# Optimization experiments

Hardware: AMD Instinct MI355X
Metric: run time of the kernel (lower is better)

Reference implementation:

```python
import jax, jax.numpy as jnp
import numpy as np

N = 50000          # nodes
E = 1_600_000      # edges
IN = 256           # in_channels
C = 32             # hidden_channels (per-head width)
HEADS = 4
BN_EPS = 1e-5


def setup_inputs() -> dict:
    key = jax.random.key(0)
    ks = jax.random.split(key, 32)
    g = lambda k, shp, s=0.1: (jax.random.normal(k, shp, jnp.float32) * s)
    inp = {
        "x": jax.random.normal(ks[0], (N, IN), jnp.float32),
        "edge_index": jax.random.randint(ks[1], (2, E), 0, N, jnp.int64),
        "edge_attr": jax.random.uniform(ks[2], (E, 1), jnp.float32),
        # conv1 (GATConv in=IN, out=C, heads=HEADS, edge_dim=1)
        "W1": g(ks[3], (IN, HEADS * C)),
        "as1": g(ks[4], (HEADS, C)),
        "ad1": g(ks[5], (HEADS, C)),
        "We1": g(ks[6], (1, HEADS * C)),
        "ae1": g(ks[7], (HEADS, C)),
        "b1": jnp.zeros((HEADS * C,), jnp.float32),
        # bn1 (eval mode, running_mean=0, running_var=1)
        "g1": jnp.ones((HEADS * C,), jnp.float32),
        "be1": jnp.zeros((HEADS * C,), jnp.float32),
        # conv2 (GATConv in=HEADS*C, out=C, heads=1, concat=False, edge_dim=1)
        "W2": g(ks[8], (HEADS * C, C)),
        "as2": g(ks[9], (1, C)),
        "ad2": g(ks[10], (1, C)),
        "We2": g(ks[11], (1, C)),
        "ae2": g(ks[12], (1, C)),
        "b2": jnp.zeros((C,), jnp.float32),
        # bn2
        "g2": jnp.ones((C,), jnp.float32),
        "be2": jnp.zeros((C,), jnp.float32),
        # classifier: Linear(C,16) -> ReLU -> Linear(16,2)
        "Wc1": g(ks[13], (C, 16)),
        "bc1": jnp.zeros((16,), jnp.float32),
        "Wc2": g(ks[14], (16, 2)),
        "bc2": jnp.zeros((2,), jnp.float32),
        "Wr1": g(ks[15], (C, 16)),
        "br1": jnp.zeros((16,), jnp.float32),
        "Wr2": g(ks[16], (16, 1)),
        "br2": jnp.zeros((1,), jnp.float32),
    }
    return inp


def _gat_conv(x, src, dst, eattr, W, a_src, a_dst, We, a_e, bias, heads, c, concat):
    n = x.shape[0]
    xs = (x @ W).reshape(n, heads, c)                       # [N,H,C]
    al_s = (xs * a_src).sum(-1)                              # [N,H]
    al_d = (xs * a_dst).sum(-1)                              # [N,H]
    ee = (eattr @ We).reshape(-1, heads, c)                  # [E,H,C]
    al_e = (ee * a_e).sum(-1)                                # [E,H]
    alpha = al_s[src] + al_d[dst] + al_e                     # [E,H]
    alpha = jax.nn.leaky_relu(alpha, 0.2)
    # segment softmax over destination node
    mx = jax.ops.segment_max(alpha, dst, num_segments=n)
    ex = jnp.exp(alpha - mx[dst])
    den = jax.ops.segment_sum(ex, dst, num_segments=n)
    a = ex / (den[dst] + 1e-16)                              # [E,H]
    out = jax.ops.segment_sum(xs[src] * a[..., None], dst, num_segments=n)  # [N,H,C]
    out = out.reshape(n, heads * c) if concat else out.mean(axis=1)
    return out + bias


def _add_self_loops(src, dst, eattr, n):
    loop = jnp.arange(n, dtype=src.dtype)
    fill = jnp.broadcast_to(eattr.mean(axis=0, keepdims=True), (n, eattr.shape[1]))
    return (jnp.concatenate([src, loop]), jnp.concatenate([dst, loop]),
            jnp.concatenate([eattr, fill], axis=0))


def _bn_eval(x, gamma, beta):
    # running_mean=0, running_var=1 (fresh BatchNorm1d, eval mode)
    return x * (gamma / jnp.sqrt(1.0 + BN_EPS)) + beta


def reference(x, edge_index, edge_attr, W1, as1, ad1, We1, ae1, b1, g1, be1,
              W2, as2, ad2, We2, ae2, b2, g2, be2,
              Wc1, bc1, Wc2, bc2, Wr1, br1, Wr2, br2):
    n = x.shape[0]
    src, dst, ea = _add_self_loops(edge_index[0], edge_index[1], edge_attr, n)
    h = _gat_conv(x, src, dst, ea, W1, as1, ad1, We1, ae1, b1, HEADS, C, True)
    h = jax.nn.elu(_bn_eval(h, g1, be1))
    h = _gat_conv(h, src, dst, ea, W2, as2, ad2, We2, ae2, b2, 1, C, False)
    h = jax.nn.elu(_bn_eval(h, g2, be2))
    cls = jax.nn.relu(h @ Wc1 + bc1) @ Wc2 + bc2             # [N,2]
    reg = (jax.nn.relu(h @ Wr1 + br1) @ Wr2 + br2)[:, 0]     # [N]
    return cls, reg, h
```

## Files before the change

### kernel.cpp

```cpp
#include <hip/hip_runtime.h>
#include <cstdint>
#include <cstddef>

#define NN 50000
#define EE 1600000
#define IN_DIM 256
#define HC 128
#define CD 32
#define BN_RS 0.9999950000374997f

#define CAP1 128
#define CAP2 128
#define NBKT 196
#define S1_B 782
#define HIST_B 320
#define G1_B 782

typedef __attribute__((ext_vector_type(8))) short short8;
typedef __attribute__((ext_vector_type(4))) float f32x4;

__device__ __forceinline__ float lrelu(float a) { return a > 0.f ? a : 0.2f * a; }
__device__ __forceinline__ float elu(float a) { return a > 0.f ? a : (__expf(a) - 1.f); }

__device__ __forceinline__ unsigned short f2bf(float f) {
    unsigned int u = __float_as_uint(f);
    unsigned int r = (u + 0x7FFFu + ((u >> 16) & 1u)) >> 16;
    return (unsigned short)r;
}
__device__ __forceinline__ float bf2f(unsigned short b) {
    return __uint_as_float(((unsigned int)b) << 16);
}
__device__ __forceinline__ float2 bf2f2(unsigned int p) {
    float2 r;
    r.x = __uint_as_float(p << 16);
    r.y = __uint_as_float(p & 0xFFFF0000u);
    return r;
}
__device__ __forceinline__ void unpack_edge(unsigned long long p, int& s, float& eav) {
    s = (int)(unsigned int)(p & 0xFFFFFFFFull);
    eav = __uint_as_float((unsigned int)(p >> 32));
}

__device__ __forceinline__ int block_excl_scan_256(int v, int tid, int* wsum) {
    int lane = tid & 63, wv = tid >> 6;
    int x = v;
    #pragma unroll
    for (int off = 1; off < 64; off <<= 1) {
        int y = __shfl_up(x, off);
        if (lane >= off) x += y;
    }
    if (lane == 63) wsum[wv] = x;
    __syncthreads();
    int wpre = 0;
    #pragma unroll
    for (int w = 0; w < 4; w++)
        if (w < wv) wpre += wsum[w];
    return wpre + x - v;
}

__global__ __launch_bounds__(256) void k0_prep(const float* __restrict__ W1,
                                               const float* __restrict__ W2,
                                               const float* __restrict__ We1,
                                               const float* __restrict__ ae1,
                                               const float* __restrict__ We2,
                                               const float* __restrict__ ae2,
                                               unsigned short* __restrict__ W1hi,
                                               unsigned short* __restrict__ W1lo,
                                               unsigned short* __restrict__ W2hi,
                                               unsigned short* __restrict__ W2lo,
                                               float* __restrict__ consts,
                                               int* __restrict__ bucketHist) {
    int blk = blockIdx.x;
    int tid = threadIdx.x;
    if (blk < 16) {
        int t = blk * 256 + tid;
        int lane = t & 63;
        int kt = (t >> 6) & 7;
        int nt = t >> 9;
        int kbase = kt * 32 + (lane >> 4) * 8;
        int col = nt * 16 + (lane & 15);
        size_t obase = (size_t)t * 8;
        #pragma unroll
        for (int j = 0; j < 8; j++) {
            float w = W1[(size_t)(kbase + j) * HC + col];
            unsigned short h = f2bf(w);
            W1hi[obase + j] = h;
            W1lo[obase + j] = f2bf(w - bf2f(h));
        }
    } else if (blk < 18) {
        int t = (blk - 16) * 256 + tid;
        int lane = t & 63;
        int kt = (t >> 6) & 3;
        int nt = t >> 8;
        int kbase = kt * 32 + (lane >> 4) * 8;
        int col = nt * 16 + (lane & 15);
        size_t obase = (size_t)t * 8;
        #pragma unroll
        for (int j = 0; j < 8; j++) {
            float w = W2[(size_t)(kbase + j) * CD + col];
            unsigned short h = f2bf(w);
            W2hi[obase + j] = h;
            W2lo[obase + j] = f2bf(w - bf2f(h));
        }
    } else {
        if (tid < NBKT) bucketHist[tid] = 0;
        if (tid == 200) consts[0] = 0.f;
        if (tid < 4) {
            float s = 0.f;
            for (int c = 0; c < 32; c++) s += We1[tid * 32 + c] * ae1[tid * 32 + c];
            consts[2 + tid] = s;
        } else if (tid == 4) {
            float s = 0.f;
            for (int c = 0; c < 32; c++) s += We2[c] * ae2[c];
            consts[6] = s;
        }
    }
}

__global__ __launch_bounds__(256) void kA_hist_gemm1(const int* __restrict__ ei,
                                                     const float* __restrict__ ea,
                                                     const float* __restrict__ x,
                                                     const unsigned short* __restrict__ Whi,
                                                     const unsigned short* __restrict__ Wlo,
                                                     int* __restrict__ bucketHist,
                                                     float* __restrict__ easum,
                                                     unsigned short* __restrict__ xs1b) {
    __shared__ int h[256];
    int tid = threadIdx.x;
    if (blockIdx.x < HIST_B) {
        h[tid] = 0;
        __syncthreads();
        float s = 0.f;
        for (int i = blockIdx.x * 256 + tid; i < EE; i += HIST_B * 256) {
            atomicAdd(&h[ei[EE + i] >> 8], 1);
            s += ea[i];
        }
        __syncthreads();
        if (tid < NBKT && h[tid] > 0) atomicAdd(&bucketHist[tid], h[tid]);
        #pragma unroll
        for (int off = 32; off > 0; off >>= 1) s += __shfl_xor(s, off);
        if ((tid & 63) == 0) atomicAdd(easum, s);
    } else {
        int lane = tid & 63, wv = tid >> 6;
        int row0 = (blockIdx.x - HIST_B) * 64 + wv * 16;
        if (row0 >= NN) return;
        int m = lane & 15;
        int q = lane >> 4;
        f32x4 acc[8];
        #pragma unroll
        for (int nt = 0; nt < 8; nt++) acc[nt] = {0.f, 0.f, 0.f, 0.f};
        const float* xrow = x + (size_t)(row0 + m) * IN_DIM + q * 8;
        #pragma unroll
        for (int kt = 0; kt < 8; kt++) {
            float4 v0 = *(const float4*)(xrow + kt * 32);
            float4 v1 = *(const float4*)(xrow + kt * 32 + 4);
            float vv[8] = {v0.x, v0.y, v0.z, v0.w, v1.x, v1.y, v1.z, v1.w};
            short8 ahi, alo;
            #pragma unroll
            for (int j = 0; j < 8; j++) {
                unsigned short hh = f2bf(vv[j]);
                ahi[j] = (short)hh;
                alo[j] = (short)f2bf(vv[j] - bf2f(hh));
            }
            #pragma unroll
            for (int nt = 0; nt < 8; nt++) {
                size_t fb = ((size_t)(nt * 8 + kt) * 64 + lane) * 8;
                short8 bhi = *(const short8*)(Whi + fb);
                short8 blo = *(const short8*)(Wlo + fb);
                acc[nt] = __builtin_amdgcn_mfma_f32_16x16x32_bf16(ahi, bhi, acc[nt], 0, 0, 0);
                acc[nt] = __builtin_amdgcn_mfma_f32_16x16x32_bf16(ahi, blo, acc[nt], 0, 0, 0);
                acc[nt] = __builtin_amdgcn_mfma_f32_16x16x32_bf16(alo, bhi, acc[nt], 0, 0, 0);
            }
        }
        #pragma unroll
        for (int nt = 0; nt < 8; nt++) {
            #pragma unroll
            for (int reg = 0; reg < 4; reg++) {
                int row = row0 + q * 4 + reg;
                xs1b[(size_t)row * HC + nt * 16 + m] = f2bf(acc[nt][reg]);
            }
        }
    }
}

__global__ void bucket_scan(const int* __restrict__ bucketHist,
                            int* __restrict__ bucketBase,
                            int* __restrict__ bucketCursor,
                            int* __restrict__ indptr,
                            float* __restrict__ consts) {
    __shared__ int wsum[4];
    int tid = threadIdx.x;
    int v = (tid < NBKT) ? bucketHist[tid] : 0;
    int excl = block_excl_scan_256(v, tid, wsum);
    if (tid <= NBKT) bucketBase[tid] = (tid == NBKT) ? EE : excl;
    if (tid < NBKT) bucketCursor[tid] = excl;
    if (tid == 0) { indptr[NN] = EE; consts[1] = consts[0] / (float)EE; }
}

__global__ __launch_bounds__(256) void kB_stage1_al1(const int* __restrict__ ei,
                                                     const float* __restrict__ ea,
                                                     int* __restrict__ bucketCursor,
                                                     int* __restrict__ Adst,
                                                     int* __restrict__ Asrc,
                                                     float* __restrict__ Aea,
                                                     const unsigned short* __restrict__ xs1b,
                                                     const float* __restrict__ as1,
                                                     const float* __restrict__ ad1,
                                                     float* __restrict__ als,
                                                     float* __restrict__ ald) {
    __shared__ int cnt[256];
    __shared__ int basel[256];
    __shared__ int gbase[256];
    __shared__ int wsum[4];
    __shared__ int sdst[2048];
    __shared__ int ssrc[2048];
    __shared__ float sea[2048];
    int tid = threadIdx.x;
    if (blockIdx.x < S1_B) {
        int base = blockIdx.x * 2048;
        cnt[tid] = 0;
        __syncthreads();
        int d[8], s[8], r[8], bk[8];
        float e[8];
        #pragma unroll
        for (int k = 0; k < 8; k++) {
            int i = base + k * 256 + tid;
            if (i < EE) {
                d[k] = ei[EE + i];
                s[k] = ei[i];
                e[k] = ea[i];
                bk[k] = d[k] >> 8;
                r[k] = atomicAdd(&cnt[bk[k]], 1);
            } else d[k] = -1;
        }
        __syncthreads();
        int v = cnt[tid];
        int excl = block_excl_scan_256(v, tid, wsum);
        basel[tid] = excl;
        if (tid < NBKT) gbase[tid] = atomicAdd(&bucketCursor[tid], v);
        __syncthreads();
        #pragma unroll
        for (int k = 0; k < 8; k++) {
            if (d[k] >= 0) {
                int slot = basel[bk[k]] + r[k];
                sdst[slot] = d[k];
                ssrc[slot] = s[k];
                sea[slot] = e[k];
            }
        }
        __syncthreads();
        int total = basel[255] + cnt[255];
        for (int slot = tid; slot < total; slot += 256) {
            int dd = sdst[slot];
            int b = dd >> 8;
            int pos = gbase[b] + (slot - basel[b]);
            Adst[pos] = dd;
            Asrc[pos] = ssrc[slot];
            Aea[pos] = sea[slot];
        }
    } else {
        int t = (blockIdx.x - S1_B) * 256 + tid;
        if (t < NN * 4) {
            int hh = t & 3;
            const unsigned int* xp = (const unsigned int*)(xs1b + (size_t)t * 32);
            const float* ap = as1 + hh * 32;
            const float* dp = ad1 + hh * 32;
            float s = 0.f, d = 0.f;
            #pragma unroll
            for (int q = 0; q < 16; q++) {
                float2 v = bf2f2(xp[q]);
                s += v.x * ap[q * 2] + v.y * ap[q * 2 + 1];
                d += v.x * dp[q * 2] + v.y * dp[q * 2 + 1];
            }
            als[t] = s;
            ald[t] = d;
        }
    }
}

__global__ __launch_bounds__(1024) void stage2_kernel(const int* __restrict__ bucketBase,
                                                      const int* __restrict__ Adst,
                                                      const int* __restrict__ Asrc,
                                                      const float* __restrict__ Aea,
                                                      int* __restrict__ indptr,
                                                      unsigned long long* __restrict__ edgedat) {
    __shared__ int cnt[256];
    __shared__ int dbase[256];
    int tid = threadIdx.x;
    int b = blockIdx.x;
    int start = bucketBase[b], end = bucketBase[b + 1];
    if (tid < 256) cnt[tid] = 0;
    __syncthreads();
    for (int i = start + tid; i < end; i += 1024) atomicAdd(&cnt[Adst[i] & 255], 1);
    __syncthreads();
    if (tid < 64) {
        int b4 = tid * 4;
        int c0 = cnt[b4], c1 = cnt[b4 + 1], c2 = cnt[b4 + 2], c3 = cnt[b4 + 3];
        int t = c0 + c1 + c2 + c3;
        int x = t;
        #pragma unroll
        for (int off = 1; off < 64; off <<= 1) {
            int y = __shfl_up(x, off);
            if (tid >= off) x += y;
        }
        int e0 = x - t;
        dbase[b4] = e0;
        dbase[b4 + 1] = e0 + c0;
        dbase[b4 + 2] = e0 + c0 + c1;
        dbase[b4 + 3] = e0 + c0 + c1 + c2;
    }
    __syncthreads();
    if (tid < 256) {
        int n = b * 256 + tid;
        if (n < NN) indptr[n] = start + dbase[tid];
        cnt[tid] = 0;
    }
    __syncthreads();
    for (int i = start + tid; i < end; i += 1024) {
        int dl = Adst[i] & 255;
        int r = atomicAdd(&cnt[dl], 1);
        int pos = start + dbase[dl] + r;
        edgedat[pos] = (unsigned long long)(unsigned int)Asrc[i] |
                       ((unsigned long long)__float_as_uint(Aea[i]) << 32);
    }
}

__global__ __launch_bounds__(256) void gat1_agg(
    const unsigned short* __restrict__ xs1b, const float* __restrict__ als,
    const float* __restrict__ ald, const unsigned long long* __restrict__ edgedat,
    const int* __restrict__ indptr, const float* __restrict__ consts,
    const float* __restrict__ b1, const float* __restrict__ g1,
    const float* __restrict__ be1,
    unsigned short* __restrict__ h1hi, unsigned short* __restrict__ h1lo) {
    __shared__ float exbuf[4][CAP1 * 4];
    __shared__ int srcbuf[4][CAP1];
    int wv = threadIdx.x >> 6;
    int lane = threadIdx.x & 63;
    int n = blockIdx.x * 4 + wv;
    int start = indptr[n];
    int deg = indptr[n + 1] - start;
    float ea_mean = consts[1];
    float ce[4] = {consts[2], consts[3], consts[4], consts[5]};
    float4 a4d = *(const float4*)(ald + (size_t)n * 4);
    float aldh[4] = {a4d.x, a4d.y, a4d.z, a4d.w};
    float4 a4s = *(const float4*)(als + (size_t)n * 4);
    float alsn[4] = {a4s.x, a4s.y, a4s.z, a4s.w};
    float ex0[4], sm[4];
    #pragma unroll
    for (int h = 0; h < 4; h++) {
        ex0[h] = __expf(lrelu(alsn[h] + aldh[h] + ea_mean * ce[h]));
        sm[h] = 0.f;
    }
    const unsigned long long* edp = edgedat + start;
    for (int i = lane; i < deg; i += 64) {
        int s; float eav;
        unpack_edge(edp[i], s, eav);
        float4 v4 = *(const float4*)(als + (size_t)s * 4);
        float alv[4] = {v4.x, v4.y, v4.z, v4.w};
        bool st = (i < CAP1);
        if (st) srcbuf[wv][i] = s * HC;
        #pragma unroll
        for (int h = 0; h < 4; h++) {
            float exv = __expf(lrelu(alv[h] + aldh[h] + eav * ce[h]));
            if (st) exbuf[wv][i * 4 + h] = exv;
            sm[h] += exv;
        }
    }
    #pragma unroll
    for (int h = 0; h < 4; h++)
        for (int off = 32; off > 0; off >>= 1) sm[h] += __shfl_xor(sm[h], off);
    float inv[4];
    #pragma unroll
    for (int h = 0; h < 4; h++) inv[h] = 1.0f / (sm[h] + ex0[h] + 1e-16f);
    int mcap = deg < CAP1 ? deg : CAP1;
    for (int i = lane; i < mcap; i += 64) {
        #pragma unroll
        for (int h = 0; h < 4; h++) exbuf[wv][i * 4 + h] *= inv[h];
    }
    int c = lane * 2;
    int h = lane >> 4;
    float wsl = ex0[h] * inv[h];
    float2 vself = bf2f2(*(const unsigned int*)(xs1b + (size_t)n * HC + c));
    float accx = vself.x * wsl, accy = vself.y * wsl;
    int i = 0;
    for (; i + 4 <= mcap; i += 4) {
        float w0 = exbuf[wv][(i + 0) * 4 + h];
        float w1 = exbuf[wv][(i + 1) * 4 + h];
        float w2 = exbuf[wv][(i + 2) * 4 + h];
        float w3 = exbuf[wv][(i + 3) * 4 + h];
        int o0 = srcbuf[wv][i + 0], o1 = srcbuf[wv][i + 1];
        int o2 = srcbuf[wv][i + 2], o3 = srcbuf[wv][i + 3];
        float2 v0 = bf2f2(*(const unsigned int*)(xs1b + o0 + c));
        float2 v1 = bf2f2(*(const unsigned int*)(xs1b + o1 + c));
        float2 v2 = bf2f2(*(const unsigned int*)(xs1b + o2 + c));
        float2 v3 = bf2f2(*(const unsigned int*)(xs1b + o3 + c));
        accx += v0.x * w0; accy += v0.y * w0;
        accx += v1.x * w1; accy += v1.y * w1;
        accx += v2.x * w2; accy += v2.y * w2;
        accx += v3.x * w3; accy += v3.y * w3;
    }
    for (; i < mcap; i++) {
        float w0 = exbuf[wv][i * 4 + h];
        int o0 = srcbuf[wv][i];
        float2 v0 = bf2f2(*(const unsigned int*)(xs1b + o0 + c));
        accx += v0.x * w0; accy += v0.y * w0;
    }
    for (; i < deg; i++) {
        int s; float eav;
        unpack_edge(edp[i], s, eav);
        float a = lrelu(als[(size_t)s * 4 + h] + aldh[h] + eav * ce[h]);
        float w0 = __expf(a) * inv[h];
        float2 v0 = bf2f2(*(const unsigned int*)(xs1b + (size_t)s * HC + c));
        accx += v0.x * w0; accy += v0.y * w0;
    }
    float o0 = accx + b1[c];
    float o1 = accy + b1[c + 1];
    o0 = o0 * (g1[c] * BN_RS) + be1[c];
    o1 = o1 * (g1[c + 1] * BN_RS) + be1[c + 1];
    o0 = elu(o0);
    o1 = elu(o1);
    unsigned short h0 = f2bf(o0), h1v = f2bf(o1);
    unsigned short l0 = f2bf(o0 - bf2f(h0)), l1 = f2bf(o1 - bf2f(h1v));
    *(unsigned int*)(h1hi + (size_t)n * HC + c) = (unsigned int)h0 | ((unsigned int)h1v << 16);
    *(unsigned int*)(h1lo + (size_t)n * HC + c) = (unsigned int)l0 | ((unsigned int)l1 << 16);
}

__global__ __launch_bounds__(256) void gemm2_mfma(const unsigned short* __restrict__ h1hi,
                                                  const unsigned short* __restrict__ h1lo,
                                                  const unsigned short* __restrict__ W2hi,
                                                  const unsigned short* __restrict__ W2lo,
                                                  const float* __restrict__ as2,
                                                  const float* __restrict__ ad2,
                                                  unsigned short* __restrict__ xs2b,
                                                  float* __restrict__ als2,
                                                  float* __restrict__ ald2) {
    int tid = threadIdx.x;
    int lane = tid & 63, wv = tid >> 6;
    int row0 = blockIdx.x * 64 + wv * 16;
    if (row0 >= NN) return;
    int m = lane & 15, q = lane >> 4;
    f32x4 acc[2];
    acc[0] = {0.f, 0.f, 0.f, 0.f};
    acc[1] = {0.f, 0.f, 0.f, 0.f};
    const unsigned short* rhi = h1hi + (size_t)(row0 + m) * HC + q * 8;
    const unsigned short* rlo = h1lo + (size_t)(row0 + m) * HC + q * 8;
    #pragma unroll
    for (int kt = 0; kt < 4; kt++) {
        short8 ahi = *(const short8*)(rhi + kt * 32);
        short8 alo = *(const short8*)(rlo + kt * 32);
        #pragma unroll
        for (int nt = 0; nt < 2; nt++) {
            size_t fb = ((size_t)(nt * 4 + kt) * 64 + lane) * 8;
            short8 bhi = *(const short8*)(W2hi + fb);
            short8 blo = *(const short8*)(W2lo + fb);
            acc[nt] = __builtin_amdgcn_mfma_f32_16x16x32_bf16(ahi, bhi, acc[nt], 0, 0, 0);
            acc[nt] = __builtin_amdgcn_mfma_f32_16x16x32_bf16(ahi, blo, acc[nt], 0, 0, 0);
            acc[nt] = __builtin_amdgcn_mfma_f32_16x16x32_bf16(alo, bhi, acc[nt], 0, 0, 0);
        }
    }
    float a0 = as2[m], a1 = as2[m + 16];
    float d0 = ad2[m], d1 = ad2[m + 16];
    #pragma unroll
    for (int reg = 0; reg < 4; reg++) {
        int row = row0 + q * 4 + reg;
        xs2b[(size_t)row * CD + m]      = f2bf(acc[0][reg]);
        xs2b[(size_t)row * CD + 16 + m] = f2bf(acc[1][reg]);
        float s = acc[0][reg] * a0 + acc[1][reg] * a1;
        float d = acc[0][reg] * d0 + acc[1][reg] * d1;
        #pragma unroll
        for (int off = 1; off < 16; off <<= 1) {
            s += __shfl_xor(s, off);
            d += __shfl_xor(d, off);
        }
        if (m == 0) { als2[row] = s; ald2[row] = d; }
    }
}

__global__ __launch_bounds__(256) void gat2_agg(
    const unsigned short* __restrict__ xs2b, const float* __restrict__ als,
    const float* __restrict__ ald, const unsigned long long* __restrict__ edgedat,
    const int* __restrict__ indptr, const float* __restrict__ consts,
    const float* __restrict__ b2, const float* __restrict__ g2, const float* __restrict__ be2,
    const float* __restrict__ Wc1, const float* __restrict__ bc1,
    const float* __restrict__ Wc2, const float* __restrict__ bc2,
    const float* __restrict__ Wr1, const float* __restrict__ br1,
    const float* __restrict__ Wr2, const float* __restrict__ br2,
    float* __restrict__ hout, float* __restrict__ cls, float* __restrict__ reg) {
    __shared__ float exbuf[4][CAP2];
    __shared__ int srcbuf[4][CAP2];
    __shared__ float hbuf[4][32];
    int wv = threadIdx.x >> 6;
    int lane = threadIdx.x & 63;
    int n = blockIdx.x * 4 + wv;
    int start = indptr[n];
    int deg = indptr[n + 1] - start;
    float ea_mean = consts[1];
    float ce = consts[6];
    float aldn = ald[n];
    float ex0 = __expf(lrelu(als[n] + aldn + ea_mean * ce));
    float sm = 0.f;
    const unsigned long long* edp = edgedat + start;
    for (int i = lane; i < deg; i += 64) {
        int s; float eav;
        unpack_edge(edp[i], s, eav);
        float exv = __expf(lrelu(als[s] + aldn + eav * ce));
        if (i < CAP2) { srcbuf[wv][i] = s * CD; exbuf[wv][i] = exv; }
        sm += exv;
    }
    for (int off = 32; off > 0; off >>= 1) sm += __shfl_xor(sm, off);
    float invd = 1.0f / (sm + ex0 + 1e-16f);
    int mcap = deg < CAP2 ? deg : CAP2;
    for (int i = lane; i < mcap; i += 64) exbuf[wv][i] *= invd;
    int quarter = lane >> 4;
    int cl = lane & 15;
    int c = cl * 2;
    float accx = 0.f, accy = 0.f;
    if (quarter == 0) {
        float2 vs = bf2f2(*(const unsigned int*)(xs2b + (size_t)n * CD + c));
        float wsl = ex0 * invd;
        accx = vs.x * wsl; accy = vs.y * wsl;
    }
    for (int i = quarter; i < mcap; i += 4) {
        float w0 = exbuf[wv][i];
        int o0 = srcbuf[wv][i];
        float2 v0 = bf2f2(*(const unsigned int*)(xs2b + o0 + c));
        accx += v0.x * w0; accy += v0.y * w0;
    }
    for (int i = CAP2 + quarter; i < deg; i += 4) {
        int s; float eav;
        unpack_edge(edp[i], s, eav);
        float w0 = __expf(lrelu(als[s] + aldn + eav * ce)) * invd;
        float2 v0 = bf2f2(*(const unsigned int*)(xs2b + (size_t)s * CD + c));
        accx += v0.x * w0; accy += v0.y * w0;
    }
    accx += __shfl_xor(accx, 16); accy += __shfl_xor(accy, 16);
    accx += __shfl_xor(accx, 32); accy += __shfl_xor(accy, 32);
    if (lane < 16) {
        float o0 = accx + b2[c];
        float o1 = accy + b2[c + 1];
        o0 = o0 * (g2[c] * BN_RS) + be2[c];
        o1 = o1 * (g2[c + 1] * BN_RS) + be2[c + 1];
        o0 = elu(o0);
        o1 = elu(o1);
        hbuf[wv][c] = o0;
        hbuf[wv][c + 1] = o1;
        *(float2*)(hout + (size_t)n * CD + c) = make_float2(o0, o1);
    }
    __syncthreads();
    float r0 = 0.f, r1 = 0.f;
    if (lane < 32) {
        int j = lane & 15;
        bool iscls = lane < 16;
        float s = iscls ? bc1[j] : br1[j];
        #pragma unroll
        for (int cc = 0; cc < 32; cc++) {
            float w = iscls ? Wc1[cc * 16 + j] : Wr1[cc * 16 + j];
            s += hbuf[wv][cc] * w;
        }
        s = fmaxf(s, 0.f);
        if (iscls) { r0 = s * Wc2[j * 2]; r1 = s * Wc2[j * 2 + 1]; }
        else       { r0 = s * Wr2[j]; }
    }
    #pragma unroll
    for (int off = 1; off < 16; off <<= 1) {
        r0 += __shfl_xor(r0, off);
        r1 += __shfl_xor(r1, off);
    }
    if (lane == 0)  *(float2*)(cls + (size_t)n * 2) = make_float2(r0 + bc2[0], r1 + bc2[1]);
    if (lane == 16) reg[n] = r0 + br2[0];
}

extern "C" void kernel_launch(void* const* d_in, const int* in_sizes, int n_in,
                              void* d_out, int out_size, void* d_ws, size_t ws_size,
                              hipStream_t stream) {
    const float* x   = (const float*)d_in[0];
    const int*   ei  = (const int*)d_in[1];
    const float* ea  = (const float*)d_in[2];
    const float* W1  = (const float*)d_in[3];
    const float* as1 = (const float*)d_in[4];
    const float* ad1 = (const float*)d_in[5];
    const float* We1 = (const float*)d_in[6];
    const float* ae1 = (const float*)d_in[7];
    const float* b1  = (const float*)d_in[8];
    const float* g1  = (const float*)d_in[9];
    const float* be1 = (const float*)d_in[10];
    const float* W2  = (const float*)d_in[11];
    const float* as2 = (const float*)d_in[12];
    const float* ad2 = (const float*)d_in[13];
    const float* We2 = (const float*)d_in[14];
    const float* ae2 = (const float*)d_in[15];
    const float* b2  = (const float*)d_in[16];
    const float* g2  = (const float*)d_in[17];
    const float* be2 = (const float*)d_in[18];
    const float* Wc1 = (const float*)d_in[19];
    const float* bc1 = (const float*)d_in[20];
    const float* Wc2 = (const float*)d_in[21];
    const float* bc2 = (const float*)d_in[22];
    const float* Wr1 = (const float*)d_in[23];
    const float* br1 = (const float*)d_in[24];
    const float* Wr2 = (const float*)d_in[25];
    const float* br2 = (const float*)d_in[26];

    char* ws = (char*)d_ws;
    unsigned short* xs1b = (unsigned short*)(ws + 0);
    unsigned short* h1hi = (unsigned short*)(ws + 12800000);
    unsigned short* h1lo = (unsigned short*)(ws + 25600000);
    int*   Adst          = (int*)(ws + 12800000);
    int*   Asrc          = (int*)(ws + 19200000);
    float* Aea           = (float*)(ws + 25600000);
    unsigned short* xs2b = (unsigned short*)(ws + 38400000);
    float* als1          = (float*)(ws + 41600000);
    float* ald1          = (float*)(ws + 42400000);
    float* als2          = (float*)(ws + 43200000);
    float* ald2          = (float*)(ws + 43400000);
    float* consts        = (float*)(ws + 43600000);
    int*   bucketHist    = (int*)(ws + 43600128);
    int*   bucketBase    = (int*)(ws + 43601024);
    int*   bucketCursor  = (int*)(ws + 43601920);
    int*   indptr        = (int*)(ws + 43602816);
    unsigned long long* edgedat = (unsigned long long*)(ws + 43802824);
    unsigned short* W1hi = (unsigned short*)(ws + 56602832);
    unsigned short* W1lo = (unsigned short*)(ws + 56668368);
    unsigned short* W2hi = (unsigned short*)(ws + 56733904);
    unsigned short* W2lo = (unsigned short*)(ws + 56742096);

    float* out_cls = (float*)d_out;
    float* out_reg = out_cls + 2 * NN;
    float* out_h   = out_cls + 3 * NN;

    k0_prep<<<19, 256, 0, stream>>>(W1, W2, We1, ae1, We2, ae2,
                                    W1hi, W1lo, W2hi, W2lo, consts, bucketHist);
    kA_hist_gemm1<<<HIST_B + G1_B, 256, 0, stream>>>(ei, ea, x, W1hi, W1lo,
                                                     bucketHist, consts, xs1b);
    bucket_scan<<<1, 256, 0, stream>>>(bucketHist, bucketBase, bucketCursor, indptr, consts);
    kB_stage1_al1<<<S1_B + 782, 256, 0, stream>>>(ei, ea, bucketCursor, Adst, Asrc, Aea,
                                                  xs1b, as1, ad1, als1, ald1);
    stage2_kernel<<<NBKT, 1024, 0, stream>>>(bucketBase, Adst, Asrc, Aea, indptr, edgedat);

    gat1_agg<<<NN / 4, 256, 0, stream>>>(xs1b, als1, ald1, edgedat, indptr, consts,
                                         b1, g1, be1, h1hi, h1lo);
    gemm2_mfma<<<G1_B, 256, 0, stream>>>(h1hi, h1lo, W2hi, W2lo, as2, ad2,
                                         xs2b, als2, ald2);
    gat2_agg<<<NN / 4, 256, 0, stream>>>(xs2b, als2, ald2, edgedat, indptr, consts,
                                         b2, g2, be2, Wc1, bc1, Wc2, bc2,
                                         Wr1, br1, Wr2, br2, out_h, out_cls, out_reg);
}
```

Measured before the change: 350.9 us.

## Remap GAT aggregation lanes to half-wave per node with wider gathers

gat1_agg now gives each node 32 lanes instead of a full 64-lane wave and packs 8 nodes per block. Each lane gathers 8 bytes (4 bf16 channels), the gather loop is unrolled by 8, and softmax normalisation is deferred to the accumulator so the per-edge weight rescaling pass goes away. gat2_agg splits a wave into 8 lanes per edge with 8 edges in flight, also using 8-byte gathers and deferred normalisation, and drops a block barrier. The aim is fewer gather instructions, better lane utilisation on nodes with about 33 neighbours, and more memory-level parallelism. In exchange the per-node LDS cache shrinks to 120 edges and register pressure rises from the deeper unroll.

```diff
diff --git a/kernel.cpp b/kernel.cpp
--- a/kernel.cpp
+++ b/kernel.cpp
@@ -9,7 +9,7 @@
 #define CD 32
 #define BN_RS 0.9999950000374997f
 
-#define CAP1 128
+#define CAP1 120
 #define CAP2 128
 #define NBKT 196
 #define S1_B 782
@@ -39,6 +39,9 @@
 __device__ __forceinline__ void unpack_edge(unsigned long long p, int& s, float& eav) {
     s = (int)(unsigned int)(p & 0xFFFFFFFFull);
     eav = __uint_as_float((unsigned int)(p >> 32));
+}
+__device__ __forceinline__ float pick4(float a, float b, float c, float d, int h) {
+    return (h & 2) ? ((h & 1) ? d : c) : ((h & 1) ? b : a);
 }
 
 __device__ __forceinline__ int block_excl_scan_256(int v, int tid, int* wsum) {
@@ -325,104 +328,124 @@
     }
 }
 
-__global__ __launch_bounds__(256) void gat1_agg(
+#define ACC4(vv, ww) { float2 p0_ = bf2f2((vv).x); float2 p1_ = bf2f2((vv).y); \
+    acc0 += p0_.x * (ww); acc1 += p0_.y * (ww); acc2 += p1_.x * (ww); acc3 += p1_.y * (ww); }
+
+__global__ __launch_bounds__(256, 8) void gat1_agg(
     const unsigned short* __restrict__ xs1b, const float* __restrict__ als,
     const float* __restrict__ ald, const unsigned long long* __restrict__ edgedat,
     const int* __restrict__ indptr, const float* __restrict__ consts,
     const float* __restrict__ b1, const float* __restrict__ g1,
     const float* __restrict__ be1,
     unsigned short* __restrict__ h1hi, unsigned short* __restrict__ h1lo) {
-    __shared__ float exbuf[4][CAP1 * 4];
-    __shared__ int srcbuf[4][CAP1];
-    int wv = threadIdx.x >> 6;
-    int lane = threadIdx.x & 63;
-    int n = blockIdx.x * 4 + wv;
+    __shared__ __align__(16) float exbuf[8][CAP1][4];
+    __shared__ int srcbuf[8][CAP1];
+    int tid = threadIdx.x;
+    int l = tid & 31;
+    int nb = tid >> 5;
+    int n = blockIdx.x * 8 + nb;
     int start = indptr[n];
     int deg = indptr[n + 1] - start;
     float ea_mean = consts[1];
-    float ce[4] = {consts[2], consts[3], consts[4], consts[5]};
+    float ce0 = consts[2], ce1 = consts[3], ce2 = consts[4], ce3 = consts[5];
     float4 a4d = *(const float4*)(ald + (size_t)n * 4);
-    float aldh[4] = {a4d.x, a4d.y, a4d.z, a4d.w};
     float4 a4s = *(const float4*)(als + (size_t)n * 4);
-    float alsn[4] = {a4s.x, a4s.y, a4s.z, a4s.w};
-    float ex0[4], sm[4];
-    #pragma unroll
-    for (int h = 0; h < 4; h++) {
-        ex0[h] = __expf(lrelu(alsn[h] + aldh[h] + ea_mean * ce[h]));
-        sm[h] = 0.f;
-    }
+    float ex00 = __expf(lrelu(a4s.x + a4d.x + ea_mean * ce0));
+    float ex01 = __expf(lrelu(a4s.y + a4d.y + ea_mean * ce1));
+    float ex02 = __expf(lrelu(a4s.z + a4d.z + ea_mean * ce2));
+    float ex03 = __expf(lrelu(a4s.w + a4d.w + ea_mean * ce3));
+    float sm0 = 0.f, sm1 = 0.f, sm2 = 0.f, sm3 = 0.f;
     const unsigned long long* edp = edgedat + start;
-    for (int i = lane; i < deg; i += 64) {
+    for (int i = l; i < deg; i += 32) {
         int s; float eav;
         unpack_edge(edp[i], s, eav);
         float4 v4 = *(const float4*)(als + (size_t)s * 4);
-        float alv[4] = {v4.x, v4.y, v4.z, v4.w};
-        bool st = (i < CAP1);
-        if (st) srcbuf[wv][i] = s * HC;
-        #pragma unroll
-        for (int h = 0; h < 4; h++) {
-            float exv = __expf(lrelu(alv[h] + aldh[h] + eav * ce[h]));
-            if (st) exbuf[wv][i * 4 + h] = exv;
-            sm[h] += exv;
-        }
-    }
-    #pragma unroll
-    for (int h = 0; h < 4; h++)
-        for (int off = 32; off > 0; off >>= 1) sm[h] += __shfl_xor(sm[h], off);
-    float inv[4];
-    #pragma unroll
-    for (int h = 0; h < 4; h++) inv[h] = 1.0f / (sm[h] + ex0[h] + 1e-16f);
+        float4 ex4;
+        ex4.x = __expf(lrelu(v4.x + a4d.x + eav * ce0)); sm0 += ex4.x;
+        ex4.y = __expf(lrelu(v4.y + a4d.y + eav * ce1)); sm1 += ex4.y;
+        ex4.z = __expf(lrelu(v4.z + a4d.z + eav * ce2)); sm2 += ex4.z;
+        ex4.w = __expf(lrelu(v4.w + a4d.w + eav * ce3)); sm3 += ex4.w;
+        if (i < CAP1) {
+            srcbuf[nb][i] = s * (HC * 2);
+            *(float4*)(&exbuf[nb][i][0]) = ex4;
+        }
+    }
+    #pragma unroll
+    for (int off = 16; off > 0; off >>= 1) {
+        sm0 += __shfl_xor(sm0, off);
+        sm1 += __shfl_xor(sm1, off);
+        sm2 += __shfl_xor(sm2, off);
+        sm3 += __shfl_xor(sm3, off);
+    }
+    int h2 = l >> 3;
+    float ex0sel = pick4(ex00, ex01, ex02, ex03, h2);
+    float inv = 1.0f / (pick4(sm0, sm1, sm2, sm3, h2) + ex0sel + 1e-16f);
     int mcap = deg < CAP1 ? deg : CAP1;
-    for (int i = lane; i < mcap; i += 64) {
-        #pragma unroll
-        for (int h = 0; h < 4; h++) exbuf[wv][i * 4 + h] *= inv[h];
-    }
-    int c = lane * 2;
-    int h = lane >> 4;
-    float wsl = ex0[h] * inv[h];
-    float2 vself = bf2f2(*(const unsigned int*)(xs1b + (size_t)n * HC + c));
-    float accx = vself.x * wsl, accy = vself.y * wsl;
+    const char* xb = (const char*)xs1b + (size_t)l * 8;
+    float acc0, acc1, acc2, acc3;
+    {
+        uint2 v = *(const uint2*)(xb + (size_t)n * (HC * 2));
+        float2 p0 = bf2f2(v.x), p1 = bf2f2(v.y);
+        acc0 = p0.x * ex0sel; acc1 = p0.y * ex0sel;
+        acc2 = p1.x * ex0sel; acc3 = p1.y * ex0sel;
+    }
     int i = 0;
-    for (; i + 4 <= mcap; i += 4) {
-        float w0 = exbuf[wv][(i + 0) * 4 + h];
-        float w1 = exbuf[wv][(i + 1) * 4 + h];
-        float w2 = exbuf[wv][(i + 2) * 4 + h];
-        float w3 = exbuf[wv][(i + 3) * 4 + h];
-        int o0 = srcbuf[wv][i + 0], o1 = srcbuf[wv][i + 1];
-        int o2 = srcbuf[wv][i + 2], o3 = srcbuf[wv][i + 3];
-        float2 v0 = bf2f2(*(const unsigned int*)(xs1b + o0 + c));
-        float2 v1 = bf2f2(*(const unsigned int*)(xs1b + o1 + c));
-        float2 v2 = bf2f2(*(const unsigned int*)(xs1b + o2 + c));
-        float2 v3 = bf2f2(*(const unsigned int*)(xs1b + o3 + c));
-        accx += v0.x * w0; accy += v0.y * w0;
-        accx += v1.x * w1; accy += v1.y * w1;
-        accx += v2.x * w2; accy += v2.y * w2;
-        accx += v3.x * w3; accy += v3.y * w3;
+    for (; i + 8 <= mcap; i += 8) {
+        int o0 = srcbuf[nb][i + 0], o1 = srcbuf[nb][i + 1];
+        int o2 = srcbuf[nb][i + 2], o3 = srcbuf[nb][i + 3];
+        int o4 = srcbuf[nb][i + 4], o5 = srcbuf[nb][i + 5];
+        int o6 = srcbuf[nb][i + 6], o7 = srcbuf[nb][i + 7];
+        float w0 = exbuf[nb][i + 0][h2], w1 = exbuf[nb][i + 1][h2];
+        float w2 = exbuf[nb][i + 2][h2], w3 = exbuf[nb][i + 3][h2];
+        float w4 = exbuf[nb][i + 4][h2], w5 = exbuf[nb][i + 5][h2];
+        float w6 = exbuf[nb][i + 6][h2], w7 = exbuf[nb][i + 7][h2];
+        uint2 v0 = *(const uint2*)(xb + o0);
+        uint2 v1 = *(const uint2*)(xb + o1);
+        uint2 v2 = *(const uint2*)(xb + o2);
+        uint2 v3 = *(const uint2*)(xb + o3);
+        uint2 v4 = *(const uint2*)(xb + o4);
+        uint2 v5 = *(const uint2*)(xb + o5);
+        uint2 v6 = *(const uint2*)(xb + o6);
+        uint2 v7 = *(const uint2*)(xb + o7);
+        ACC4(v0, w0); ACC4(v1, w1); ACC4(v2, w2); ACC4(v3, w3);
+        ACC4(v4, w4); ACC4(v5, w5); ACC4(v6, w6); ACC4(v7, w7);
     }
     for (; i < mcap; i++) {
-        float w0 = exbuf[wv][i * 4 + h];
-        int o0 = srcbuf[wv][i];
-        float2 v0 = bf2f2(*(const unsigned int*)(xs1b + o0 + c));
-        accx += v0.x * w0; accy += v0.y * w0;
-    }
-    for (; i < deg; i++) {
-        int s; float eav;
-        unpack_edge(edp[i], s, eav);
-        float a = lrelu(als[(size_t)s * 4 + h] + aldh[h] + eav * ce[h]);
-        float w0 = __expf(a) * inv[h];
-        float2 v0 = bf2f2(*(const unsigned int*)(xs1b + (size_t)s * HC + c));
-        accx += v0.x * w0; accy += v0.y * w0;
-    }
-    float o0 = accx + b1[c];
-    float o1 = accy + b1[c + 1];
-    o0 = o0 * (g1[c] * BN_RS) + be1[c];
-    o1 = o1 * (g1[c + 1] * BN_RS) + be1[c + 1];
-    o0 = elu(o0);
-    o1 = elu(o1);
-    unsigned short h0 = f2bf(o0), h1v = f2bf(o1);
+        int o = srcbuf[nb][i];
+        float w = exbuf[nb][i][h2];
+        uint2 v = *(const uint2*)(xb + o);
+        ACC4(v, w);
+    }
+    if (deg > CAP1) {
+        float aldsel = pick4(a4d.x, a4d.y, a4d.z, a4d.w, h2);
+        float cesel = pick4(ce0, ce1, ce2, ce3, h2);
+        for (int j = CAP1; j < deg; j++) {
+            int s; float eav;
+            unpack_edge(edp[j], s, eav);
+            float w = __expf(lrelu(als[(size_t)s * 4 + h2] + aldsel + eav * cesel));
+            uint2 v = *(const uint2*)(xb + (size_t)s * (HC * 2));
+            ACC4(v, w);
+        }
+    }
+    acc0 *= inv; acc1 *= inv; acc2 *= inv; acc3 *= inv;
+    int c = l * 4;
+    float4 bb = *(const float4*)(b1 + c);
+    float4 gg = *(const float4*)(g1 + c);
+    float4 eb = *(const float4*)(be1 + c);
+    float o0 = elu((acc0 + bb.x) * (gg.x * BN_RS) + eb.x);
+    float o1 = elu((acc1 + bb.y) * (gg.y * BN_RS) + eb.y);
+    float o2 = elu((acc2 + bb.z) * (gg.z * BN_RS) + eb.z);
+    float o3 = elu((acc3 + bb.w) * (gg.w * BN_RS) + eb.w);
+    unsigned short h0 = f2bf(o0), h1v = f2bf(o1), h2v = f2bf(o2), h3v = f2bf(o3);
     unsigned short l0 = f2bf(o0 - bf2f(h0)), l1 = f2bf(o1 - bf2f(h1v));
-    *(unsigned int*)(h1hi + (size_t)n * HC + c) = (unsigned int)h0 | ((unsigned int)h1v << 16);
-    *(unsigned int*)(h1lo + (size_t)n * HC + c) = (unsigned int)l0 | ((unsigned int)l1 << 16);
+    unsigned short l2 = f2bf(o2 - bf2f(h2v)), l3 = f2bf(o3 - bf2f(h3v));
+    uint2 hiw, low;
+    hiw.x = (unsigned int)h0 | ((unsigned int)h1v << 16);
+    hiw.y = (unsigned int)h2v | ((unsigned int)h3v << 16);
+    low.x = (unsigned int)l0 | ((unsigned int)l1 << 16);
+    low.y = (unsigned int)l2 | ((unsigned int)l3 << 16);
+    *(uint2*)(h1hi + (size_t)n * HC + c) = hiw;
+    *(uint2*)(h1lo + (size_t)n * HC + c) = low;
 }
 
 __global__ __launch_bounds__(256) void gemm2_mfma(const unsigned short* __restrict__ h1hi,
@@ -488,7 +511,7 @@
     float* __restrict__ hout, float* __restrict__ cls, float* __restrict__ reg) {
     __shared__ float exbuf[4][CAP2];
     __shared__ int srcbuf[4][CAP2];
-    __shared__ float hbuf[4][32];
+    __shared__ __align__(16) float hbuf[4][32];
     int wv = threadIdx.x >> 6;
     int lane = threadIdx.x & 63;
     int n = blockIdx.x * 4 + wv;
@@ -504,49 +527,53 @@
         int s; float eav;
         unpack_edge(edp[i], s, eav);
         float exv = __expf(lrelu(als[s] + aldn + eav * ce));
-        if (i < CAP2) { srcbuf[wv][i] = s * CD; exbuf[wv][i] = exv; }
+        if (i < CAP2) { srcbuf[wv][i] = s * (CD * 2); exbuf[wv][i] = exv; }
         sm += exv;
     }
+    #pragma unroll
     for (int off = 32; off > 0; off >>= 1) sm += __shfl_xor(sm, off);
     float invd = 1.0f / (sm + ex0 + 1e-16f);
     int mcap = deg < CAP2 ? deg : CAP2;
-    for (int i = lane; i < mcap; i += 64) exbuf[wv][i] *= invd;
-    int quarter = lane >> 4;
-    int cl = lane & 15;
-    int c = cl * 2;
-    float accx = 0.f, accy = 0.f;
-    if (quarter == 0) {
-        float2 vs = bf2f2(*(const unsigned int*)(xs2b + (size_t)n * CD + c));
-        float wsl = ex0 * invd;
-        accx = vs.x * wsl; accy = vs.y * wsl;
-    }
-    for (int i = quarter; i < mcap; i += 4) {
-        float w0 = exbuf[wv][i];
-        int o0 = srcbuf[wv][i];
-        float2 v0 = bf2f2(*(const unsigned int*)(xs2b + o0 + c));
-        accx += v0.x * w0; accy += v0.y * w0;
-    }
-    for (int i = CAP2 + quarter; i < deg; i += 4) {
+    int oct = lane >> 3, lo = lane & 7;
+    const char* xb = (const char*)xs2b + (size_t)lo * 8;
+    float acc0 = 0.f, acc1 = 0.f, acc2 = 0.f, acc3 = 0.f;
+    if (oct == 0) {
+        uint2 v = *(const uint2*)(xb + (size_t)n * (CD * 2));
+        float2 p0 = bf2f2(v.x), p1 = bf2f2(v.y);
+        acc0 = p0.x * ex0; acc1 = p0.y * ex0; acc2 = p1.x * ex0; acc3 = p1.y * ex0;
+    }
+    for (int i = oct; i < mcap; i += 8) {
+        float w = exbuf[wv][i];
+        int o = srcbuf[wv][i];
+        uint2 v = *(const uint2*)(xb + o);
+        ACC4(v, w);
+    }
+    for (int i = CAP2 + oct; i < deg; i += 8) {
         int s; float eav;
         unpack_edge(edp[i], s, eav);
-        float w0 = __expf(lrelu(als[s] + aldn + eav * ce)) * invd;
-        float2 v0 = bf2f2(*(const unsigned int*)(xs2b + (size_t)s * CD + c));
-        accx += v0.x * w0; accy += v0.y * w0;
-    }
-    accx += __shfl_xor(accx, 16); accy += __shfl_xor(accy, 16);
-    accx += __shfl_xor(accx, 32); accy += __shfl_xor(accy, 32);
-    if (lane < 16) {
-        float o0 = accx + b2[c];
-        float o1 = accy + b2[c + 1];
-        o0 = o0 * (g2[c] * BN_RS) + be2[c];
-        o1 = o1 * (g2[c + 1] * BN_RS) + be2[c + 1];
-        o0 = elu(o0);
-        o1 = elu(o1);
-        hbuf[wv][c] = o0;
-        hbuf[wv][c + 1] = o1;
-        *(float2*)(hout + (size_t)n * CD + c) = make_float2(o0, o1);
-    }
-    __syncthreads();
+        float w = __expf(lrelu(als[s] + aldn + eav * ce));
+        uint2 v = *(const uint2*)(xb + (size_t)s * (CD * 2));
+        ACC4(v, w);
+    }
+    #pragma unroll
+    for (int off = 8; off < 64; off <<= 1) {
+        acc0 += __shfl_xor(acc0, off);
+        acc1 += __shfl_xor(acc1, off);
+        acc2 += __shfl_xor(acc2, off);
+        acc3 += __shfl_xor(acc3, off);
+    }
+    if (lane < 8) {
+        int c = lo * 4;
+        float4 bb = *(const float4*)(b2 + c);
+        float4 gg = *(const float4*)(g2 + c);
+        float4 eb = *(const float4*)(be2 + c);
+        float o0 = elu((acc0 * invd + bb.x) * (gg.x * BN_RS) + eb.x);
+        float o1 = elu((acc1 * invd + bb.y) * (gg.y * BN_RS) + eb.y);
+        float o2 = elu((acc2 * invd + bb.z) * (gg.z * BN_RS) + eb.z);
+        float o3 = elu((acc3 * invd + bb.w) * (gg.w * BN_RS) + eb.w);
+        *(float4*)(&hbuf[wv][c]) = make_float4(o0, o1, o2, o3);
+        *(float4*)(hout + (size_t)n * CD + c) = make_float4(o0, o1, o2, o3);
+    }
     float r0 = 0.f, r1 = 0.f;
     if (lane < 32) {
         int j = lane & 15;
@@ -637,7 +664,7 @@
                                                   xs1b, as1, ad1, als1, ald1);
     stage2_kernel<<<NBKT, 1024, 0, stream>>>(bucketBase, Adst, Asrc, Aea, indptr, edgedat);
 
-    gat1_agg<<<NN / 4, 256, 0, stream>>>(xs1b, als1, ald1, edgedat, indptr, consts,
+    gat1_agg<<<NN / 8, 256, 0, stream>>>(xs1b, als1, ald1, edgedat, indptr, consts,
                                          b1, g1, be1, h1hi, h1lo);
     gemm2_mfma<<<G1_B, 256, 0, stream>>>(h1hi, h1lo, W2hi, W2lo, as2, ad2,
                                          xs2b, als2, ald2);
```

Result: faster. 340.1 us (-3.1%).
